# Performance work log

Hardware: AMD Instinct MI355X
Metric: run time of the kernel (lower is better)

Reference implementation:

```python
import jax, jax.numpy as jnp
import numpy as np

B, C, H, W = 16, 256, 64, 64
DIM = 8
HEADS = C // DIM          # 32
TD = HEADS * DIM          # 256 (total_dim)
EPS = 1e-15
BN_EPS = 1e-5


def setup_inputs() -> dict:
    key = jax.random.key(0)
    ks = jax.random.split(key, 7)
    s = 0.05
    return {
        "x": jax.random.normal(ks[0], (B, C, H, W), jnp.float32),
        "w_qkv": jax.random.normal(ks[1], (3 * TD, C), jnp.float32) * s,
        "w_dw": jax.random.normal(ks[2], (3 * TD, 1, 5, 5), jnp.float32) * s,
        "w_pw": jax.random.normal(ks[3], (3 * TD, DIM), jnp.float32) * s,
        "w_proj": jax.random.normal(ks[4], (C, 2 * TD), jnp.float32) * s,
        "bn_gamma": jnp.ones((C,), jnp.float32),
        "bn_beta": jnp.zeros((C,), jnp.float32),
        "bn_mean": jax.random.normal(ks[5], (C,), jnp.float32) * 0.1,
        "bn_var": jax.random.uniform(ks[6], (C,), jnp.float32, 0.5, 1.5),
    }


def reference(x, w_qkv, w_dw, w_pw, w_proj, bn_gamma, bn_beta, bn_mean, bn_var):
    # qkv: 1x1 conv, no bias -> (B, 3*TD, H, W)
    qkv = jnp.einsum('bchw,oc->bohw', x, w_qkv)

    # multi-scale aggregation: 5x5 depthwise conv then grouped 1x1 conv (groups = 3*HEADS)
    dw = jax.lax.conv_general_dilated(
        qkv, w_dw, window_strides=(1, 1), padding=[(2, 2), (2, 2)],
        dimension_numbers=('NCHW', 'OIHW', 'NCHW'), feature_group_count=3 * TD)
    G = 3 * HEADS                                   # groups; DIM channels per group
    dwg = dw.reshape(B, G, DIM, H, W)
    wg = w_pw.reshape(G, DIM, DIM)                  # (group, out_per_group, in_per_group)
    agg = jnp.einsum('bgihw,goi->bgohw', dwg, wg).reshape(B, 3 * TD, H, W)

    qkv_ms = jnp.concatenate([qkv, agg], axis=1)    # (B, 6*TD, H, W)

    # ReLU linear attention (H*W > dim branch)
    h2 = qkv_ms.shape[1] // (3 * DIM)               # 2*HEADS effective heads
    t = qkv_ms.reshape(B, h2, 3 * DIM, H * W)
    q = jax.nn.relu(t[:, :, :DIM])                  # (B,h2,DIM,N)
    k = jax.nn.relu(t[:, :, DIM:2 * DIM])           # (B,h2,DIM,N)
    v = t[:, :, 2 * DIM:]                           # (B,h2,DIM,N)
    v = jnp.concatenate([v, jnp.ones_like(v[:, :, :1])], axis=2)  # pad ones row -> (B,h2,DIM+1,N)

    vk = jnp.einsum('bhen,bhdn->bhed', v, k)        # (B,h2,DIM+1,DIM)
    out = jnp.einsum('bhed,bhdn->bhen', vk, q)      # (B,h2,DIM+1,N)
    out = out[:, :, :-1] / (out[:, :, -1:] + EPS)   # normalize by padded-ones channel
    out = out.reshape(B, h2 * DIM, H, W)            # (B, 2*TD, H, W)

    # proj: 1x1 conv + BatchNorm (inference stats)
    y = jnp.einsum('bchw,oc->bohw', out, w_proj)
    scale = (bn_gamma / jnp.sqrt(bn_var + BN_EPS))[None, :, None, None]
    y = (y - bn_mean[None, :, None, None]) * scale + bn_beta[None, :, None, None]

    return x + y
```

## Files before the change

### kernel.cpp

```cpp
#include <hip/hip_runtime.h>

#define BB 16
#define CC 256
#define HW 4096
#define TD3 768
#define TD2 512
#define WQ_N (TD3 * CC)
#define WP_N (CC * TD2)

typedef __bf16 bf16x8 __attribute__((ext_vector_type(8)));
typedef float f32x4 __attribute__((ext_vector_type(4)));
typedef const __attribute__((address_space(1))) unsigned int glb_u32;
typedef __attribute__((address_space(3))) unsigned int lds_u32;

__device__ inline ushort f2bf(float f) {
    union { float f; uint u; } v; v.f = f;
    uint u = v.u;
    return (ushort)((u + 0x7FFFu + ((u >> 16) & 1u)) >> 16);
}
__device__ inline float bf2f(ushort h) {
    union { uint u; float f; } v; v.u = ((uint)h) << 16;
    return v.f;
}
__device__ inline uint pack2(float a, float b) {
    return (uint)f2bf(a) | ((uint)f2bf(b) << 16);
}

__launch_bounds__(256)
__global__ void k_prep(const float* __restrict__ w_qkv, const float* __restrict__ w_proj,
                       ushort* __restrict__ wq_hi, ushort* __restrict__ wq_lo,
                       ushort* __restrict__ wp_hi, ushort* __restrict__ wp_lo) {
    int i = blockIdx.x * 256 + threadIdx.x;
    if (i < WQ_N) {
        float f = w_qkv[i];
        ushort h = f2bf(f);
        wq_hi[i] = h;
        wq_lo[i] = f2bf(f - bf2f(h));
    }
    if (i < WP_N) {
        float f = w_proj[i];
        ushort h = f2bf(f);
        wp_hi[i] = h;
        wp_lo[i] = f2bf(f - bf2f(h));
    }
}

__launch_bounds__(256)
__global__ void k0_transpose(const float* __restrict__ x, ushort* __restrict__ x_cl) {
    __shared__ float tile[64][65];
    int b = blockIdx.z;
    int n0 = blockIdx.x * 64;
    int c0 = blockIdx.y * 64;
    int t = threadIdx.x;
    const float* xp = x + ((size_t)b * CC + c0) * HW + n0;
    int nl = t & 63;
    int cl0 = t >> 6;
#pragma unroll
    for (int i = 0; i < 16; i++) {
        int cl = cl0 + i * 4;
        tile[cl][nl] = xp[(size_t)cl * HW + nl];
    }
    __syncthreads();
#pragma unroll
    for (int it = 0; it < 2; it++) {
        int item = t + it * 256;
        int n = item >> 3;
        int cc = item & 7;
        uint4 o;
        o.x = pack2(tile[cc * 8 + 0][n], tile[cc * 8 + 1][n]);
        o.y = pack2(tile[cc * 8 + 2][n], tile[cc * 8 + 3][n]);
        o.z = pack2(tile[cc * 8 + 4][n], tile[cc * 8 + 5][n]);
        o.w = pack2(tile[cc * 8 + 6][n], tile[cc * 8 + 7][n]);
        *(uint4*)(x_cl + ((size_t)b * HW + n0 + n) * CC + c0 + cc * 8) = o;
    }
}

__launch_bounds__(256)
__global__ void k1_qkv(const ushort* __restrict__ x_cl, const ushort* __restrict__ wq_hi,
                       const ushort* __restrict__ wq_lo, ushort* __restrict__ qk_pl,
                       float* __restrict__ v_pl) {
    __shared__ ushort Ald[128][32];
    __shared__ ushort Bh[128][32];
    __shared__ ushort Bl[128][32];
    int b = blockIdx.z;
    int n0 = blockIdx.x * 128;
    int o0 = blockIdx.y * 128;
    int t = threadIdx.x;
    int w = t >> 6, l = t & 63;
    int wn = (w >> 1) * 64, wo = (w & 1) * 64;
    f32x4 acc[4][4];
#pragma unroll
    for (int m = 0; m < 4; m++)
#pragma unroll
        for (int o = 0; o < 4; o++)
#pragma unroll
            for (int r = 0; r < 4; r++) acc[m][o][r] = 0.f;

    const ushort* Ap  = x_cl + ((size_t)b * HW + n0) * CC;
    const ushort* Bph = wq_hi + (size_t)o0 * CC;
    const ushort* Bpl = wq_lo + (size_t)o0 * CC;
    int rowl = (l >> 2);
    int coll = (l & 3) * 8;

    for (int k0 = 0; k0 < CC; k0 += 32) {
#pragma unroll
        for (int i = 0; i < 2; i++) {
            int rbase = w * 32 + i * 16;
            int row = rbase + rowl;
            __builtin_amdgcn_global_load_lds((glb_u32*)(Ap + (size_t)row * CC + k0 + coll),
                                             (lds_u32*)&Ald[rbase][0], 16, 0, 0);
            __builtin_amdgcn_global_load_lds((glb_u32*)(Bph + (size_t)row * CC + k0 + coll),
                                             (lds_u32*)&Bh[rbase][0], 16, 0, 0);
            __builtin_amdgcn_global_load_lds((glb_u32*)(Bpl + (size_t)row * CC + k0 + coll),
                                             (lds_u32*)&Bl[rbase][0], 16, 0, 0);
        }
        __syncthreads();
        bf16x8 af[4], bh[4], bl[4];
#pragma unroll
        for (int m = 0; m < 4; m++) af[m] = *(const bf16x8*)&Ald[wn + m * 16 + (l & 15)][(l >> 4) * 8];
#pragma unroll
        for (int o = 0; o < 4; o++) {
            bh[o] = *(const bf16x8*)&Bh[wo + o * 16 + (l & 15)][(l >> 4) * 8];
            bl[o] = *(const bf16x8*)&Bl[wo + o * 16 + (l & 15)][(l >> 4) * 8];
        }
#pragma unroll
        for (int m = 0; m < 4; m++)
#pragma unroll
            for (int o = 0; o < 4; o++) {
                acc[m][o] = __builtin_amdgcn_mfma_f32_16x16x32_bf16(af[m], bh[o], acc[m][o], 0, 0, 0);
                acc[m][o] = __builtin_amdgcn_mfma_f32_16x16x32_bf16(af[m], bl[o], acc[m][o], 0, 0, 0);
            }
        __syncthreads();
    }
#pragma unroll
    for (int m = 0; m < 4; m++) {
        int nb = n0 + wn + m * 16 + (l >> 4) * 4;
#pragma unroll
        for (int oi = 0; oi < 4; oi++) {
            int o = o0 + wo + oi * 16 + (l & 15);
            int hl = o / 24;
            int r = o - hl * 24;
            if (r < 16) {
                uint2 pv;
                pv.x = pack2(acc[m][oi][0], acc[m][oi][1]);
                pv.y = pack2(acc[m][oi][2], acc[m][oi][3]);
                *(uint2*)(qk_pl + ((size_t)b * 1024 + hl * 16 + r) * HW + nb) = pv;
            } else {
                float4 v4 = {acc[m][oi][0], acc[m][oi][1], acc[m][oi][2], acc[m][oi][3]};
                *(float4*)(v_pl + ((size_t)b * 512 + hl * 8 + (r - 16)) * HW + nb) = v4;
            }
        }
    }
}

__launch_bounds__(256)
__global__ void k2_dwpw(const ushort* __restrict__ qk_pl, const float* __restrict__ v_pl,
                        const float* __restrict__ w_dw, const float* __restrict__ w_pw) {
    __shared__ __align__(16) char ldsraw[2 * 36 * 76 * 4];
    int g = blockIdx.x;
    int strip = blockIdx.y;
    int b = blockIdx.z;
    int t = threadIdx.x;
    int y0 = strip * 32;
    int hl = g / 3, tau = g % 3;
    const float* wg  = w_dw + (size_t)g * 200;
    const float* wpg = w_pw + (size_t)g * 64;
    int rp = t >> 4;
    int seg = t & 15;

    float ag[8][8];
#pragma unroll
    for (int o = 0; o < 8; o++)
#pragma unroll
        for (int j = 0; j < 8; j++) ag[o][j] = 0.f;

    if (tau < 2) {
        typedef ushort (*ltile_t)[36][72];
        ltile_t lds = (ltile_t)ldsraw;
        const ushort* src = qk_pl + ((size_t)b * 1024 + hl * 16 + tau * 8) * HW;
        ushort* dst = (ushort*)qk_pl + ((size_t)b * 1024 + 512 + hl * 16 + tau * 8) * HW;
        if (t < 72) {
            int ch = t / 36, row = t - ch * 36;
            *(uint*)(&lds[ch][row][0]) = 0u;
            *(uint*)(&lds[ch][row][66]) = 0u;
        }
#pragma unroll 1
        for (int cp = 0; cp < 4; cp++) {
            if (cp) __syncthreads();
#pragma unroll
            for (int i = 0; i < 3; i++) {
                int slot = t + i * 256;
                if (slot < 576) {
                    int ch = slot / 288;
                    int rem = slot - ch * 288;
                    int row = rem >> 3;
                    int q = rem & 7;
                    int yy = y0 - 2 + row;
                    uint4 v = {0u, 0u, 0u, 0u};
                    if (yy >= 0 && yy < 64)
                        v = *(const uint4*)(src + (size_t)(2 * cp + ch) * HW + yy * 64 + q * 8);
                    ushort* rowp = &lds[ch][row][2 + q * 8];
                    *(uint*)(rowp + 0) = v.x; *(uint*)(rowp + 2) = v.y;
                    *(uint*)(rowp + 4) = v.z; *(uint*)(rowp + 6) = v.w;
                }
            }
            __syncthreads();
#pragma unroll
            for (int ch = 0; ch < 2; ch++) {
                int c = cp * 2 + ch;
                float dw0[4] = {0.f, 0.f, 0.f, 0.f};
                float dw1[4] = {0.f, 0.f, 0.f, 0.f};
#pragma unroll
                for (int j = 0; j < 6; j++) {
                    ushort4 wa = *(const ushort4*)&lds[ch][rp * 2 + j][4 * seg];
                    ushort4 wb = *(const ushort4*)&lds[ch][rp * 2 + j][4 * seg + 4];
                    float win[8];
                    win[0] = bf2f(wa.x); win[1] = bf2f(wa.y); win[2] = bf2f(wa.z); win[3] = bf2f(wa.w);
                    win[4] = bf2f(wb.x); win[5] = bf2f(wb.y); win[6] = bf2f(wb.z); win[7] = bf2f(wb.w);
                    if (j <= 4) {
#pragma unroll
                        for (int dx = 0; dx < 5; dx++) {
                            float wv = wg[c * 25 + j * 5 + dx];
#pragma unroll
                            for (int k = 0; k < 4; k++) dw0[k] += win[dx + k] * wv;
                        }
                    }
                    if (j >= 1) {
#pragma unroll
                        for (int dx = 0; dx < 5; dx++) {
                            float wv = wg[c * 25 + (j - 1) * 5 + dx];
#pragma unroll
                            for (int k = 0; k < 4; k++) dw1[k] += win[dx + k] * wv;
                        }
                    }
                }
#pragma unroll
                for (int o = 0; o < 8; o++) {
                    float wv = wpg[o * 8 + c];
#pragma unroll
                    for (int k = 0; k < 4; k++) {
                        ag[o][k] += dw0[k] * wv;
                        ag[o][4 + k] += dw1[k] * wv;
                    }
                }
            }
        }
        int n0 = (y0 + rp * 2) * 64 + seg * 4;
#pragma unroll
        for (int o = 0; o < 8; o++) {
            uint2 r0, r1;
            r0.x = pack2(ag[o][0], ag[o][1]); r0.y = pack2(ag[o][2], ag[o][3]);
            r1.x = pack2(ag[o][4], ag[o][5]); r1.y = pack2(ag[o][6], ag[o][7]);
            *(uint2*)(dst + (size_t)o * HW + n0) = r0;
            *(uint2*)(dst + (size_t)o * HW + n0 + 64) = r1;
        }
    } else {
        typedef float (*ltile_t)[36][76];
        ltile_t lds = (ltile_t)ldsraw;
        const float* src = v_pl + ((size_t)b * 512 + hl * 8) * HW;
        float* dst = (float*)v_pl + ((size_t)b * 512 + 256 + hl * 8) * HW;
        if (t < 144) {
            int ch = t / 72, rem = t - ch * 72;
            int row = rem >> 1, side = rem & 1;
            float2 z2 = {0.f, 0.f};
            *(float2*)(&lds[ch][row][side ? 66 : 0]) = z2;
        }
#pragma unroll 1
        for (int cp = 0; cp < 4; cp++) {
            if (cp) __syncthreads();
#pragma unroll
            for (int i = 0; i < 5; i++) {
                int slot = t + i * 256;
                if (slot < 1152) {
                    int ch = slot / 576;
                    int rem = slot - ch * 576;
                    int row = rem >> 4;
                    int q = rem & 15;
                    int yy = y0 - 2 + row;
                    float4 v = {0.f, 0.f, 0.f, 0.f};
                    if (yy >= 0 && yy < 64)
                        v = *(const float4*)(src + (size_t)(2 * cp + ch) * HW + yy * 64 + q * 4);
                    float2 lo2 = {v.x, v.y}, hi2 = {v.z, v.w};
                    *(float2*)(&lds[ch][row][2 + 4 * q]) = lo2;
                    *(float2*)(&lds[ch][row][4 + 4 * q]) = hi2;
                }
            }
            __syncthreads();
#pragma unroll
            for (int ch = 0; ch < 2; ch++) {
                int c = cp * 2 + ch;
                float dw0[4] = {0.f, 0.f, 0.f, 0.f};
                float dw1[4] = {0.f, 0.f, 0.f, 0.f};
#pragma unroll
                for (int j = 0; j < 6; j++) {
                    float win[8];
                    *(float4*)&win[0] = *(const float4*)&lds[ch][rp * 2 + j][4 * seg];
                    *(float4*)&win[4] = *(const float4*)&lds[ch][rp * 2 + j][4 * seg + 4];
                    if (j <= 4) {
#pragma unroll
                        for (int dx = 0; dx < 5; dx++) {
                            float wv = wg[c * 25 + j * 5 + dx];
#pragma unroll
                            for (int k = 0; k < 4; k++) dw0[k] += win[dx + k] * wv;
                        }
                    }
                    if (j >= 1) {
#pragma unroll
                        for (int dx = 0; dx < 5; dx++) {
                            float wv = wg[c * 25 + (j - 1) * 5 + dx];
#pragma unroll
                            for (int k = 0; k < 4; k++) dw1[k] += win[dx + k] * wv;
                        }
                    }
                }
#pragma unroll
                for (int o = 0; o < 8; o++) {
                    float wv = wpg[o * 8 + c];
#pragma unroll
                    for (int k = 0; k < 4; k++) {
                        ag[o][k] += dw0[k] * wv;
                        ag[o][4 + k] += dw1[k] * wv;
                    }
                }
            }
        }
        int n0 = (y0 + rp * 2) * 64 + seg * 4;
#pragma unroll
        for (int o = 0; o < 8; o++) {
            float4 r0 = {ag[o][0], ag[o][1], ag[o][2], ag[o][3]};
            float4 r1 = {ag[o][4], ag[o][5], ag[o][6], ag[o][7]};
            *(float4*)(dst + (size_t)o * HW + n0) = r0;
            *(float4*)(dst + (size_t)o * HW + n0 + 64) = r1;
        }
    }
}

__launch_bounds__(256)
__global__ void k3_vk(const ushort* __restrict__ qk_pl, const float* __restrict__ v_pl,
                      float* __restrict__ vk_buf) {
    __shared__ float vk_partial[4][72];
    int h = blockIdx.x;
    int b = blockIdx.y;
    int s = blockIdx.z;
    const ushort* kp = qk_pl + ((size_t)b * 1024 + (h >> 5) * 512 + (h & 31) * 16 + 8) * HW;
    const float*  vp = v_pl  + ((size_t)b * 512  + (h >> 5) * 256 + (h & 31) * 8) * HW;
    int t = threadIdx.x;
    float vk[9][8];
#pragma unroll
    for (int e = 0; e < 9; e++)
#pragma unroll
        for (int d = 0; d < 8; d++) vk[e][d] = 0.f;

#pragma unroll
    for (int it = 0; it < 2; it++) {
        int n4 = s * 2048 + (t + it * 256) * 4;
        float4 kf[8], vf[8];
#pragma unroll
        for (int d = 0; d < 8; d++) {
            ushort4 ku = *(const ushort4*)(kp + (size_t)d * HW + n4);
            kf[d].x = fmaxf(bf2f(ku.x), 0.f); kf[d].y = fmaxf(bf2f(ku.y), 0.f);
            kf[d].z = fmaxf(bf2f(ku.z), 0.f); kf[d].w = fmaxf(bf2f(ku.w), 0.f);
        }
#pragma unroll
        for (int e = 0; e < 8; e++) vf[e] = *(const float4*)(vp + (size_t)e * HW + n4);
#pragma unroll
        for (int e = 0; e < 8; e++)
#pragma unroll
            for (int d = 0; d < 8; d++)
                vk[e][d] += vf[e].x * kf[d].x + vf[e].y * kf[d].y + vf[e].z * kf[d].z + vf[e].w * kf[d].w;
#pragma unroll
        for (int d = 0; d < 8; d++) vk[8][d] += kf[d].x + kf[d].y + kf[d].z + kf[d].w;
    }
#pragma unroll
    for (int e = 0; e < 9; e++)
#pragma unroll
        for (int d = 0; d < 8; d++) {
            float v = vk[e][d];
            for (int off = 32; off > 0; off >>= 1) v += __shfl_xor(v, off);
            vk[e][d] = v;
        }
    int w = t >> 6, l = t & 63;
    if (l == 0) {
#pragma unroll
        for (int e = 0; e < 9; e++)
#pragma unroll
            for (int d = 0; d < 8; d++) vk_partial[w][e * 8 + d] = vk[e][d];
    }
    __syncthreads();
    if (t < 72) {
        float sum = vk_partial[0][t] + vk_partial[1][t] + vk_partial[2][t] + vk_partial[3][t];
        vk_buf[(((size_t)b * 64 + h) * 2 + s) * 72 + t] = sum;
    }
}

__launch_bounds__(256)
__global__ void k3_out(const ushort* __restrict__ qk_pl, const float* __restrict__ vk_buf,
                       ushort* __restrict__ out_cl) {
    __shared__ float vk_s[72];
    int h = blockIdx.x;
    int b = blockIdx.y;
    int s = blockIdx.z;
    const ushort* qp = qk_pl + ((size_t)b * 1024 + (h >> 5) * 512 + (h & 31) * 16) * HW;
    int t = threadIdx.x;
    if (t < 72) {
        const float* vb = vk_buf + ((size_t)b * 64 + h) * 2 * 72 + t;
        vk_s[t] = vb[0] + vb[72];
    }
    __syncthreads();
    float vkf[9][8];
#pragma unroll
    for (int e = 0; e < 9; e++)
#pragma unroll
        for (int d = 0; d < 8; d++) vkf[e][d] = vk_s[e * 8 + d];

    int n4 = s * 1024 + t * 4;
    float qa[4][8];
#pragma unroll
    for (int d = 0; d < 8; d++) {
        ushort4 qu = *(const ushort4*)(qp + (size_t)d * HW + n4);
        qa[0][d] = fmaxf(bf2f(qu.x), 0.f); qa[1][d] = fmaxf(bf2f(qu.y), 0.f);
        qa[2][d] = fmaxf(bf2f(qu.z), 0.f); qa[3][d] = fmaxf(bf2f(qu.w), 0.f);
    }
    ushort* dst = out_cl + (size_t)b * HW * TD2 + h * 8;
#pragma unroll
    for (int j = 0; j < 4; j++) {
        float o[9];
#pragma unroll
        for (int e = 0; e < 9; e++) {
            float sum = 0.f;
#pragma unroll
            for (int d = 0; d < 8; d++) sum += vkf[e][d] * qa[j][d];
            o[e] = sum;
        }
        float inv = 1.f / (o[8] + 1e-15f);
        uint4 ov;
        ov.x = pack2(o[0] * inv, o[1] * inv); ov.y = pack2(o[2] * inv, o[3] * inv);
        ov.z = pack2(o[4] * inv, o[5] * inv); ov.w = pack2(o[6] * inv, o[7] * inv);
        *(uint4*)(dst + (size_t)(n4 + j) * TD2) = ov;
    }
}

__launch_bounds__(256)
__global__ void k4_proj(const ushort* __restrict__ out_cl, const ushort* __restrict__ wp_hi,
                        const ushort* __restrict__ wp_lo, const float* __restrict__ x,
                        const float* __restrict__ gamma, const float* __restrict__ beta,
                        const float* __restrict__ mean, const float* __restrict__ var_,
                        float* __restrict__ out) {
    __shared__ ushort Ah[128][32];
    __shared__ ushort Al[128][32];
    __shared__ ushort Bld[128][32];
    int b = blockIdx.z;
    int n0 = blockIdx.x * 128;
    int c0 = blockIdx.y * 128;
    int t = threadIdx.x;
    int w = t >> 6, l = t & 63;
    int wc = (w >> 1) * 64, wn = (w & 1) * 64;
    f32x4 acc[4][4];
#pragma unroll
    for (int m = 0; m < 4; m++)
#pragma unroll
        for (int o = 0; o < 4; o++)
#pragma unroll
            for (int r = 0; r < 4; r++) acc[m][o][r] = 0.f;

    const ushort* Aph = wp_hi + (size_t)c0 * TD2;
    const ushort* Apl = wp_lo + (size_t)c0 * TD2;
    const ushort* Bp  = out_cl + ((size_t)b * HW + n0) * TD2;
    int rowl = (l >> 2);
    int coll = (l & 3) * 8;

    for (int k0 = 0; k0 < TD2; k0 += 32) {
#pragma unroll
        for (int i = 0; i < 2; i++) {
            int rbase = w * 32 + i * 16;
            int row = rbase + rowl;
            __builtin_amdgcn_global_load_lds((glb_u32*)(Aph + (size_t)row * TD2 + k0 + coll),
                                             (lds_u32*)&Ah[rbase][0], 16, 0, 0);
            __builtin_amdgcn_global_load_lds((glb_u32*)(Apl + (size_t)row * TD2 + k0 + coll),
                                             (lds_u32*)&Al[rbase][0], 16, 0, 0);
            __builtin_amdgcn_global_load_lds((glb_u32*)(Bp + (size_t)row * TD2 + k0 + coll),
                                             (lds_u32*)&Bld[rbase][0], 16, 0, 0);
        }
        __syncthreads();
        bf16x8 ah[4], al[4], bf[4];
#pragma unroll
        for (int m = 0; m < 4; m++) {
            ah[m] = *(const bf16x8*)&Ah[wc + m * 16 + (l & 15)][(l >> 4) * 8];
            al[m] = *(const bf16x8*)&Al[wc + m * 16 + (l & 15)][(l >> 4) * 8];
        }
#pragma unroll
        for (int ni = 0; ni < 4; ni++) bf[ni] = *(const bf16x8*)&Bld[wn + ni * 16 + (l & 15)][(l >> 4) * 8];
#pragma unroll
        for (int m = 0; m < 4; m++)
#pragma unroll
            for (int ni = 0; ni < 4; ni++) {
                acc[m][ni] = __builtin_amdgcn_mfma_f32_16x16x32_bf16(ah[m], bf[ni], acc[m][ni], 0, 0, 0);
                acc[m][ni] = __builtin_amdgcn_mfma_f32_16x16x32_bf16(al[m], bf[ni], acc[m][ni], 0, 0, 0);
            }
        __syncthreads();
    }
#pragma unroll
    for (int m = 0; m < 4; m++) {
        int cb = c0 + wc + m * 16 + (l >> 4) * 4;
        float sc[4], mn[4], bt[4];
#pragma unroll
        for (int r = 0; r < 4; r++) {
            sc[r] = gamma[cb + r] * rsqrtf(var_[cb + r] + 1e-5f);
            mn[r] = mean[cb + r];
            bt[r] = beta[cb + r];
        }
#pragma unroll
        for (int ni = 0; ni < 4; ni++) {
            int n = n0 + wn + ni * 16 + (l & 15);
#pragma unroll
            for (int r = 0; r < 4; r++) {
                size_t idx = ((size_t)b * CC + cb + r) * HW + n;
                out[idx] = x[idx] + (acc[m][ni][r] - mn[r]) * sc[r] + bt[r];
            }
        }
    }
}

extern "C" void kernel_launch(void* const* d_in, const int* in_sizes, int n_in,
                              void* d_out, int out_size, void* d_ws, size_t ws_size,
                              hipStream_t stream) {
    const float* x      = (const float*)d_in[0];
    const float* w_qkv  = (const float*)d_in[1];
    const float* w_dw   = (const float*)d_in[2];
    const float* w_pw   = (const float*)d_in[3];
    const float* w_proj = (const float*)d_in[4];
    const float* gamma  = (const float*)d_in[5];
    const float* beta   = (const float*)d_in[6];
    const float* mean   = (const float*)d_in[7];
    const float* var_   = (const float*)d_in[8];
    float* out = (float*)d_out;

    const size_t static_bytes = ((size_t)WQ_N + WP_N) * 2 * 2;
    const size_t per_batch = (size_t)HW * CC * 2 + (size_t)1024 * HW * 2 + (size_t)512 * HW * 4
                           + (size_t)HW * TD2 * 2 + (size_t)64 * 2 * 72 * 4;
    size_t avail = ws_size > static_bytes ? ws_size - static_bytes : 0;
    int cb = 16;
    while (cb > 1 && (size_t)cb * per_batch > avail) cb >>= 1;

    char* ws = (char*)d_ws;
    ushort* x_cl  = (ushort*)ws;
    ushort* qk_pl = (ushort*)(ws + (size_t)cb * HW * CC * 2);
    float*  v_pl  = (float*)(ws + (size_t)cb * HW * CC * 2 + (size_t)cb * 1024 * HW * 2);
    ushort* out_cl = (ushort*)(ws + (size_t)cb * HW * CC * 2 + (size_t)cb * 1024 * HW * 2
                                  + (size_t)cb * 512 * HW * 4);
    float*  vk_buf = (float*)(ws + (size_t)cb * HW * CC * 2 + (size_t)cb * 1024 * HW * 2
                                 + (size_t)cb * 512 * HW * 4 + (size_t)cb * HW * TD2 * 2);
    char* wsw = ws + (size_t)cb * per_batch;
    ushort* wq_hi = (ushort*)wsw;
    ushort* wq_lo = wq_hi + WQ_N;
    ushort* wp_hi = wq_lo + WQ_N;
    ushort* wp_lo = wp_hi + WP_N;

    k_prep<<<dim3((WQ_N + 255) / 256), 256, 0, stream>>>(w_qkv, w_proj, wq_hi, wq_lo, wp_hi, wp_lo);

    for (int b0 = 0; b0 < BB; b0 += cb) {
        const float* xc = x + (size_t)b0 * CC * HW;
        float* oc = out + (size_t)b0 * CC * HW;
        k0_transpose<<<dim3(64, 4, cb), 256, 0, stream>>>(xc, x_cl);
        k1_qkv<<<dim3(32, 6, cb), 256, 0, stream>>>(x_cl, wq_hi, wq_lo, qk_pl, v_pl);
        k2_dwpw<<<dim3(96, 2, cb), 256, 0, stream>>>(qk_pl, v_pl, w_dw, w_pw);
        k3_vk<<<dim3(64, cb, 2), 256, 0, stream>>>(qk_pl, v_pl, vk_buf);
        k3_out<<<dim3(64, cb, 4), 256, 0, stream>>>(qk_pl, vk_buf, out_cl);
        k4_proj<<<dim3(32, 2, cb), 256, 0, stream>>>(out_cl, wp_hi, wp_lo, xc, gamma, beta, mean, var_, oc);
    }
}
```

Baseline: 391.1 us.

## Replace LDS-tiled depthwise conv with direct global window loads and finer strips

The fused depthwise 5x5 plus grouped pointwise kernel no longer stages input tiles in shared memory and no longer synchronises per channel pair. Each thread now loads its 5-row by 8-column window straight from global memory and computes one output row instead of two. The grid doubles to 4 strips per image to keep the same total work. This removes LDS traffic and barriers and lowers register use, but it relies on L1/L2 to absorb the redundant halo reads across neighbouring threads. It also issues unaligned vector loads at the row edges.

```diff
diff --git a/kernel.cpp b/kernel.cpp
--- a/kernel.cpp
+++ b/kernel.cpp
@@ -154,183 +154,112 @@
 }
 
 __launch_bounds__(256)
-__global__ void k2_dwpw(const ushort* __restrict__ qk_pl, const float* __restrict__ v_pl,
+__global__ void k2_dwpw(ushort* __restrict__ qk_pl, float* __restrict__ v_pl,
                         const float* __restrict__ w_dw, const float* __restrict__ w_pw) {
-    __shared__ __align__(16) char ldsraw[2 * 36 * 76 * 4];
     int g = blockIdx.x;
     int strip = blockIdx.y;
     int b = blockIdx.z;
     int t = threadIdx.x;
-    int y0 = strip * 32;
+    int seg = t & 15, row = t >> 4;
+    int y = strip * 16 + row;
     int hl = g / 3, tau = g % 3;
     const float* wg  = w_dw + (size_t)g * 200;
     const float* wpg = w_pw + (size_t)g * 64;
-    int rp = t >> 4;
-    int seg = t & 15;
-
-    float ag[8][8];
+
+    float ag[8][4];
 #pragma unroll
     for (int o = 0; o < 8; o++)
 #pragma unroll
-        for (int j = 0; j < 8; j++) ag[o][j] = 0.f;
+        for (int k = 0; k < 4; k++) ag[o][k] = 0.f;
+
+    int xbase = 4 * seg - 2;
 
     if (tau < 2) {
-        typedef ushort (*ltile_t)[36][72];
-        ltile_t lds = (ltile_t)ldsraw;
         const ushort* src = qk_pl + ((size_t)b * 1024 + hl * 16 + tau * 8) * HW;
-        ushort* dst = (ushort*)qk_pl + ((size_t)b * 1024 + 512 + hl * 16 + tau * 8) * HW;
-        if (t < 72) {
-            int ch = t / 36, row = t - ch * 36;
-            *(uint*)(&lds[ch][row][0]) = 0u;
-            *(uint*)(&lds[ch][row][66]) = 0u;
-        }
+        ushort* dst = qk_pl + ((size_t)b * 1024 + 512 + hl * 16 + tau * 8) * HW;
 #pragma unroll 1
-        for (int cp = 0; cp < 4; cp++) {
-            if (cp) __syncthreads();
-#pragma unroll
-            for (int i = 0; i < 3; i++) {
-                int slot = t + i * 256;
-                if (slot < 576) {
-                    int ch = slot / 288;
-                    int rem = slot - ch * 288;
-                    int row = rem >> 3;
-                    int q = rem & 7;
-                    int yy = y0 - 2 + row;
-                    uint4 v = {0u, 0u, 0u, 0u};
-                    if (yy >= 0 && yy < 64)
-                        v = *(const uint4*)(src + (size_t)(2 * cp + ch) * HW + yy * 64 + q * 8);
-                    ushort* rowp = &lds[ch][row][2 + q * 8];
-                    *(uint*)(rowp + 0) = v.x; *(uint*)(rowp + 2) = v.y;
-                    *(uint*)(rowp + 4) = v.z; *(uint*)(rowp + 6) = v.w;
+        for (int c = 0; c < 8; c++) {
+            float dw[4] = {0.f, 0.f, 0.f, 0.f};
+            float win[5][8];
+#pragma unroll
+            for (int j = 0; j < 5; j++) {
+                int yy = y - 2 + j;
+#pragma unroll
+                for (int i = 0; i < 8; i++) win[j][i] = 0.f;
+                if (yy >= 0 && yy < 64) {
+                    ushort4 wa = *(const ushort4*)(src + (size_t)c * HW + yy * 64 + xbase);
+                    ushort4 wb = *(const ushort4*)(src + (size_t)c * HW + yy * 64 + xbase + 4);
+                    win[j][0] = bf2f(wa.x); win[j][1] = bf2f(wa.y);
+                    win[j][2] = bf2f(wa.z); win[j][3] = bf2f(wa.w);
+                    win[j][4] = bf2f(wb.x); win[j][5] = bf2f(wb.y);
+                    win[j][6] = bf2f(wb.z); win[j][7] = bf2f(wb.w);
+                    if (seg == 0)  { win[j][0] = 0.f; win[j][1] = 0.f; }
+                    if (seg == 15) { win[j][6] = 0.f; win[j][7] = 0.f; }
                 }
             }
-            __syncthreads();
-#pragma unroll
-            for (int ch = 0; ch < 2; ch++) {
-                int c = cp * 2 + ch;
-                float dw0[4] = {0.f, 0.f, 0.f, 0.f};
-                float dw1[4] = {0.f, 0.f, 0.f, 0.f};
-#pragma unroll
-                for (int j = 0; j < 6; j++) {
-                    ushort4 wa = *(const ushort4*)&lds[ch][rp * 2 + j][4 * seg];
-                    ushort4 wb = *(const ushort4*)&lds[ch][rp * 2 + j][4 * seg + 4];
-                    float win[8];
-                    win[0] = bf2f(wa.x); win[1] = bf2f(wa.y); win[2] = bf2f(wa.z); win[3] = bf2f(wa.w);
-                    win[4] = bf2f(wb.x); win[5] = bf2f(wb.y); win[6] = bf2f(wb.z); win[7] = bf2f(wb.w);
-                    if (j <= 4) {
-#pragma unroll
-                        for (int dx = 0; dx < 5; dx++) {
-                            float wv = wg[c * 25 + j * 5 + dx];
-#pragma unroll
-                            for (int k = 0; k < 4; k++) dw0[k] += win[dx + k] * wv;
-                        }
-                    }
-                    if (j >= 1) {
-#pragma unroll
-                        for (int dx = 0; dx < 5; dx++) {
-                            float wv = wg[c * 25 + (j - 1) * 5 + dx];
-#pragma unroll
-                            for (int k = 0; k < 4; k++) dw1[k] += win[dx + k] * wv;
-                        }
-                    }
+#pragma unroll
+            for (int j = 0; j < 5; j++)
+#pragma unroll
+                for (int dx = 0; dx < 5; dx++) {
+                    float wv = wg[c * 25 + j * 5 + dx];
+#pragma unroll
+                    for (int k = 0; k < 4; k++) dw[k] += win[j][dx + k] * wv;
                 }
 #pragma unroll
-                for (int o = 0; o < 8; o++) {
-                    float wv = wpg[o * 8 + c];
-#pragma unroll
-                    for (int k = 0; k < 4; k++) {
-                        ag[o][k] += dw0[k] * wv;
-                        ag[o][4 + k] += dw1[k] * wv;
-                    }
+            for (int o = 0; o < 8; o++) {
+                float wv = wpg[o * 8 + c];
+#pragma unroll
+                for (int k = 0; k < 4; k++) ag[o][k] += dw[k] * wv;
+            }
+        }
+        int n = y * 64 + seg * 4;
+#pragma unroll
+        for (int o = 0; o < 8; o++) {
+            uint2 r0;
+            r0.x = pack2(ag[o][0], ag[o][1]); r0.y = pack2(ag[o][2], ag[o][3]);
+            *(uint2*)(dst + (size_t)o * HW + n) = r0;
+        }
+    } else {
+        const float* src = v_pl + ((size_t)b * 512 + hl * 8) * HW;
+        float* dst = v_pl + ((size_t)b * 512 + 256 + hl * 8) * HW;
+#pragma unroll 1
+        for (int c = 0; c < 8; c++) {
+            float dw[4] = {0.f, 0.f, 0.f, 0.f};
+            float win[5][8];
+#pragma unroll
+            for (int j = 0; j < 5; j++) {
+                int yy = y - 2 + j;
+#pragma unroll
+                for (int i = 0; i < 8; i++) win[j][i] = 0.f;
+                if (yy >= 0 && yy < 64) {
+                    float4 wa = *(const float4*)(src + (size_t)c * HW + yy * 64 + xbase);
+                    float4 wb = *(const float4*)(src + (size_t)c * HW + yy * 64 + xbase + 4);
+                    win[j][0] = wa.x; win[j][1] = wa.y; win[j][2] = wa.z; win[j][3] = wa.w;
+                    win[j][4] = wb.x; win[j][5] = wb.y; win[j][6] = wb.z; win[j][7] = wb.w;
+                    if (seg == 0)  { win[j][0] = 0.f; win[j][1] = 0.f; }
+                    if (seg == 15) { win[j][6] = 0.f; win[j][7] = 0.f; }
                 }
             }
-        }
-        int n0 = (y0 + rp * 2) * 64 + seg * 4;
-#pragma unroll
-        for (int o = 0; o < 8; o++) {
-            uint2 r0, r1;
-            r0.x = pack2(ag[o][0], ag[o][1]); r0.y = pack2(ag[o][2], ag[o][3]);
-            r1.x = pack2(ag[o][4], ag[o][5]); r1.y = pack2(ag[o][6], ag[o][7]);
-            *(uint2*)(dst + (size_t)o * HW + n0) = r0;
-            *(uint2*)(dst + (size_t)o * HW + n0 + 64) = r1;
-        }
-    } else {
-        typedef float (*ltile_t)[36][76];
-        ltile_t lds = (ltile_t)ldsraw;
-        const float* src = v_pl + ((size_t)b * 512 + hl * 8) * HW;
-        float* dst = (float*)v_pl + ((size_t)b * 512 + 256 + hl * 8) * HW;
-        if (t < 144) {
-            int ch = t / 72, rem = t - ch * 72;
-            int row = rem >> 1, side = rem & 1;
-            float2 z2 = {0.f, 0.f};
-            *(float2*)(&lds[ch][row][side ? 66 : 0]) = z2;
-        }
-#pragma unroll 1
-        for (int cp = 0; cp < 4; cp++) {
-            if (cp) __syncthreads();
-#pragma unroll
-            for (int i = 0; i < 5; i++) {
-                int slot = t + i * 256;
-                if (slot < 1152) {
-                    int ch = slot / 576;
-                    int rem = slot - ch * 576;
-                    int row = rem >> 4;
-                    int q = rem & 15;
-                    int yy = y0 - 2 + row;
-                    float4 v = {0.f, 0.f, 0.f, 0.f};
-                    if (yy >= 0 && yy < 64)
-                        v = *(const float4*)(src + (size_t)(2 * cp + ch) * HW + yy * 64 + q * 4);
-                    float2 lo2 = {v.x, v.y}, hi2 = {v.z, v.w};
-                    *(float2*)(&lds[ch][row][2 + 4 * q]) = lo2;
-                    *(float2*)(&lds[ch][row][4 + 4 * q]) = hi2;
+#pragma unroll
+            for (int j = 0; j < 5; j++)
+#pragma unroll
+                for (int dx = 0; dx < 5; dx++) {
+                    float wv = wg[c * 25 + j * 5 + dx];
+#pragma unroll
+                    for (int k = 0; k < 4; k++) dw[k] += win[j][dx + k] * wv;
                 }
-            }
-            __syncthreads();
-#pragma unroll
-            for (int ch = 0; ch < 2; ch++) {
-                int c = cp * 2 + ch;
-                float dw0[4] = {0.f, 0.f, 0.f, 0.f};
-                float dw1[4] = {0.f, 0.f, 0.f, 0.f};
-#pragma unroll
-                for (int j = 0; j < 6; j++) {
-                    float win[8];
-                    *(float4*)&win[0] = *(const float4*)&lds[ch][rp * 2 + j][4 * seg];
-                    *(float4*)&win[4] = *(const float4*)&lds[ch][rp * 2 + j][4 * seg + 4];
-                    if (j <= 4) {
-#pragma unroll
-                        for (int dx = 0; dx < 5; dx++) {
-                            float wv = wg[c * 25 + j * 5 + dx];
-#pragma unroll
-                            for (int k = 0; k < 4; k++) dw0[k] += win[dx + k] * wv;
-                        }
-                    }
-                    if (j >= 1) {
-#pragma unroll
-                        for (int dx = 0; dx < 5; dx++) {
-                            float wv = wg[c * 25 + (j - 1) * 5 + dx];
-#pragma unroll
-                            for (int k = 0; k < 4; k++) dw1[k] += win[dx + k] * wv;
-                        }
-                    }
-                }
-#pragma unroll
-                for (int o = 0; o < 8; o++) {
-                    float wv = wpg[o * 8 + c];
-#pragma unroll
-                    for (int k = 0; k < 4; k++) {
-                        ag[o][k] += dw0[k] * wv;
-                        ag[o][4 + k] += dw1[k] * wv;
-                    }
-                }
-            }
-        }
-        int n0 = (y0 + rp * 2) * 64 + seg * 4;
+#pragma unroll
+            for (int o = 0; o < 8; o++) {
+                float wv = wpg[o * 8 + c];
+#pragma unroll
+                for (int k = 0; k < 4; k++) ag[o][k] += dw[k] * wv;
+            }
+        }
+        int n = y * 64 + seg * 4;
 #pragma unroll
         for (int o = 0; o < 8; o++) {
             float4 r0 = {ag[o][0], ag[o][1], ag[o][2], ag[o][3]};
-            float4 r1 = {ag[o][4], ag[o][5], ag[o][6], ag[o][7]};
-            *(float4*)(dst + (size_t)o * HW + n0) = r0;
-            *(float4*)(dst + (size_t)o * HW + n0 + 64) = r1;
+            *(float4*)(dst + (size_t)o * HW + n) = r0;
         }
     }
 }
@@ -563,7 +492,7 @@
         float* oc = out + (size_t)b0 * CC * HW;
         k0_transpose<<<dim3(64, 4, cb), 256, 0, stream>>>(xc, x_cl);
         k1_qkv<<<dim3(32, 6, cb), 256, 0, stream>>>(x_cl, wq_hi, wq_lo, qk_pl, v_pl);
-        k2_dwpw<<<dim3(96, 2, cb), 256, 0, stream>>>(qk_pl, v_pl, w_dw, w_pw);
+        k2_dwpw<<<dim3(96, 4, cb), 256, 0, stream>>>(qk_pl, v_pl, w_dw, w_pw);
         k3_vk<<<dim3(64, cb, 2), 256, 0, stream>>>(qk_pl, v_pl, vk_buf);
         k3_out<<<dim3(64, cb, 4), 256, 0, stream>>>(qk_pl, vk_buf, out_cl);
         k4_proj<<<dim3(32, 2, cb), 256, 0, stream>>>(out_cl, wp_hi, wp_lo, xc, gamma, beta, mean, var_, oc);
```

Result: slower. 410.4 us (+4.9%).
